# Optimization experiments

Measured on AMD Instinct MI355X. Metric: run time of the kernel, lower is better.

## Reference

```python
import jax, jax.numpy as jnp
import numpy as np

NUM_EXPERTS = 8
PHM_DIM = 4


def setup_inputs() -> dict:
    key = jax.random.key(0)
    k1, k2, k3, k4 = jax.random.split(key, 4)
    bsz, seq, D, O, E, p = 4, 2048, 2048, 2048, NUM_EXPERTS, PHM_DIM
    hidden_states = jax.random.normal(k1, (bsz, seq, D), dtype=jnp.float32)
    gate_w = jax.random.normal(k2, (D, E), dtype=jnp.float32) * 0.02
    phm_rule = jax.random.normal(k3, (E, p, p, p), dtype=jnp.float32) * 0.1
    W = jax.random.normal(k4, (E, p, D // p, O // p), dtype=jnp.float32) * 0.02
    b = jnp.zeros((E, O), dtype=jnp.float32)
    return {"hidden_states": hidden_states, "gate_w": gate_w,
            "phm_rule": phm_rule, "W": W, "b": b}


def reference(hidden_states, gate_w, phm_rule, W, b):
    bsz, seq, dim = hidden_states.shape
    E = gate_w.shape[1]
    x = hidden_states.reshape(-1, dim)                      # [T, D]
    logits = x @ gate_w                                     # [T, E]
    prob = jax.nn.softmax(logits, axis=-1)                  # [T, E]
    gate = jnp.argmax(prob, axis=-1)                        # [T]
    # load-balancing loss
    num_tokens = jnp.sum(jax.nn.one_hot(gate, E, dtype=jnp.int32), axis=0)  # [E]
    f = num_tokens.astype(prob.dtype)
    f = f / jnp.sum(f)
    P = jnp.mean(prob, axis=0)
    balance_loss = E * jnp.sum(P * f)
    # PHM weight per expert: H_e = sum_p kron(phm_rule[e,p], W[e,p]) -> [E, D, O]
    Wfull = jnp.einsum('epab,epij->eaibj', phm_rule, W).reshape(E, dim, -1)
    # dense evaluation of every expert on every token, then top-1 select
    all_out = jnp.einsum('td,edo->teo', x, Wfull) + b[None, :, :]  # [T, E, O]
    tok_prob = jnp.take_along_axis(prob, gate[:, None], axis=1)    # [T, 1]
    out = jnp.take_along_axis(all_out, gate[:, None, None], axis=1)[:, 0, :] * tok_prob
    out = out.reshape(bsz, seq, -1)
    return out, balance_loss, num_tokens
```

## Files before the change

### kernel.cpp

```cpp
#include <hip/hip_runtime.h>
#include <cstdint>
#include <cstddef>

typedef _Float16 f16;
typedef f16 f16x2 __attribute__((ext_vector_type(2)));
typedef f16 f16x4 __attribute__((ext_vector_type(4)));
typedef f16 f16x8 __attribute__((ext_vector_type(8)));
typedef float f32x4 __attribute__((ext_vector_type(4)));

#define NEXP 8
#define BM 128
#define BN 128
#define BK 32

__device__ __forceinline__ void async_cp16(void* lds, const void* gsrc) {
  __builtin_amdgcn_global_load_lds(
      (const __attribute__((address_space(1))) void*)gsrc,
      (__attribute__((address_space(3))) void*)lds, 16, 0, 0);
}

__global__ __launch_bounds__(256) void k_gate(
    const float* __restrict__ x, const float* __restrict__ gw,
    f16* __restrict__ xb, int* __restrict__ gate, float* __restrict__ scale,
    int* __restrict__ cnt, float* __restrict__ probsum, int D)
{
  __shared__ float ps[NEXP];
  __shared__ int pc[NEXP];
  int tid = threadIdx.x, lane = tid & 63, w = tid >> 6;
  if (tid < NEXP) { ps[tid] = 0.f; pc[tid] = 0; }
  __syncthreads();

  int t = blockIdx.x * 4 + w;
  const float* xr = x + (size_t)t * D;
  f16* xbr = xb + (size_t)t * D;

  float acc[NEXP] = {};
  for (int d0 = lane * 4; d0 < D; d0 += 256) {
    float4 v = *(const float4*)(xr + d0);
    f16x4 h; h[0] = (f16)v.x; h[1] = (f16)v.y; h[2] = (f16)v.z; h[3] = (f16)v.w;
    *(f16x4*)(xbr + d0) = h;
    const float* g0 = gw + (size_t)d0 * NEXP;
    float xv[4] = {v.x, v.y, v.z, v.w};
#pragma unroll
    for (int j = 0; j < 4; j++) {
      float4 ga = *(const float4*)(g0 + j * NEXP);
      float4 gb = *(const float4*)(g0 + j * NEXP + 4);
      acc[0] += xv[j] * ga.x; acc[1] += xv[j] * ga.y;
      acc[2] += xv[j] * ga.z; acc[3] += xv[j] * ga.w;
      acc[4] += xv[j] * gb.x; acc[5] += xv[j] * gb.y;
      acc[6] += xv[j] * gb.z; acc[7] += xv[j] * gb.w;
    }
  }
#pragma unroll
  for (int e = 0; e < NEXP; e++) {
    float v = acc[e];
    for (int o = 32; o > 0; o >>= 1) v += __shfl_xor(v, o);
    acc[e] = v;
  }
  if (lane == 0) {
    float m = acc[0]; int g = 0;
#pragma unroll
    for (int e = 1; e < NEXP; e++) if (acc[e] > m) { m = acc[e]; g = e; }
    float pr[NEXP]; float ssum = 0.f;
#pragma unroll
    for (int e = 0; e < NEXP; e++) { pr[e] = expf(acc[e] - m); ssum += pr[e]; }
    float inv = 1.0f / ssum;
#pragma unroll
    for (int e = 0; e < NEXP; e++) atomicAdd(&ps[e], pr[e] * inv);
    atomicAdd(&pc[g], 1);
    gate[t] = g;
    scale[t] = pr[g] * inv;
  }
  __syncthreads();
  if (tid < NEXP) {
    atomicAdd(&probsum[tid], ps[tid]);
    atomicAdd(&cnt[tid], pc[tid]);
  }
}

__global__ __launch_bounds__(256) void k_wfull(
    const float* __restrict__ Wp, const float* __restrict__ rule,
    f16* __restrict__ wt, int Dp, int Op, int D, int O)
{
  int bid = blockIdx.x;
  int it = Dp >> 5, jt = Op >> 5;
  int itile = bid % it; bid /= it;
  int jtile = bid % jt; bid /= jt;
  int b = bid & 3; bid >>= 2;
  int e = bid;
  int i0 = itile * 32, j0 = jtile * 32;

  __shared__ float Wt[4][32][33];
  int tid = threadIdx.x;
  for (int idx = tid; idx < 4096; idx += 256) {
    int p = idx >> 10, rem = idx & 1023, ii = rem >> 5, jj = rem & 31;
    Wt[p][ii][jj] = Wp[(size_t)((e * 4 + p) * Dp + i0 + ii) * Op + j0 + jj];
  }
  float s[4][4];
#pragma unroll
  for (int p = 0; p < 4; p++)
#pragma unroll
    for (int a = 0; a < 4; a++)
      s[p][a] = rule[((e * 4 + p) * 4 + a) * 4 + b];
  __syncthreads();

  int ii = (tid & 15) * 2, jjb = tid >> 4;
#pragma unroll
  for (int a = 0; a < 4; a++) {
#pragma unroll
    for (int jp = 0; jp < 2; jp++) {
      int jj = jjb + jp * 16;
      float v0 = 0.f, v1 = 0.f;
#pragma unroll
      for (int p = 0; p < 4; p++) {
        v0 += s[p][a] * Wt[p][ii][jj];
        v1 += s[p][a] * Wt[p][ii + 1][jj];
      }
      size_t n = (size_t)b * Op + j0 + jj;
      size_t dd = (size_t)a * Dp + i0 + ii;
      f16x2 hv; hv[0] = (f16)v0; hv[1] = (f16)v1;
      *(f16x2*)(wt + ((size_t)e * O + n) * D + dd) = hv;
    }
  }
}

__global__ void k_plan(const int* __restrict__ cnt, const float* __restrict__ probsum,
                       int* __restrict__ offs, int* __restrict__ ndesc,
                       int2* __restrict__ desc, float* __restrict__ otail, int T)
{
  if (threadIdx.x != 0 || blockIdx.x != 0) return;
  int off = 0, nd = 0; float loss = 0.f;
  for (int e = 0; e < NEXP; e++) {
    offs[e] = off;
    int c = cnt[e];
    loss += probsum[e] * (float)c;
    for (int m0 = 0; m0 < c; m0 += BM) { desc[nd] = make_int2(e, m0); nd++; }
    off += c;
  }
  offs[NEXP] = off;
  *ndesc = nd;
  float invT = 1.0f / (float)T;
  otail[0] = (float)NEXP * loss * invT * invT;
  for (int e = 0; e < NEXP; e++) otail[1 + e] = (float)cnt[e];
}

__global__ __launch_bounds__(256) void k_scatter(
    const int* __restrict__ gate, const int* __restrict__ offs,
    int* __restrict__ cursor, int* __restrict__ perm)
{
  int t = blockIdx.x * 256 + threadIdx.x;
  int g = gate[t];
  int lane = threadIdx.x & 63;
  int pos = 0;
#pragma unroll
  for (int e = 0; e < NEXP; e++) {
    unsigned long long mask = __ballot(g == e);
    if (mask == 0ull) continue;
    int leader = __ffsll((unsigned long long)mask) - 1;
    int base = 0;
    if (lane == leader) base = atomicAdd(&cursor[e], (int)__popcll(mask));
    base = __shfl(base, leader);
    if (g == e) {
      int below = (int)__popcll(mask & ((1ull << lane) - 1ull));
      pos = offs[e] + base + below;
    }
  }
  perm[pos] = t;
}

__global__ __launch_bounds__(256) void k_gemm(
    const f16* __restrict__ xb, const f16* __restrict__ wt,
    const float* __restrict__ bias, const int* __restrict__ perm,
    const int* __restrict__ cnt, const int* __restrict__ offs,
    const int* __restrict__ ndesc, const int2* __restrict__ desc,
    const float* __restrict__ scale, float* __restrict__ out, int D, int O)
{
  if ((int)blockIdx.x >= *ndesc) return;
  int2 dsc = desc[blockIdx.x];
  int e = dsc.x, m0 = dsc.y;
  int ce = cnt[e];
  int seg = offs[e];
  int n0 = blockIdx.y * BN;

  __shared__ f16 Al[BM * BK];
  __shared__ f16 Bl[BN * BK];
  __shared__ int tokS[BM];
  __shared__ float scS[BM];

  int tid = threadIdx.x;
  if (tid < BM) {
    int idx = m0 + tid; if (idx > ce - 1) idx = ce - 1;
    int tok = perm[seg + idx];
    tokS[tid] = tok;
    scS[tid] = scale[tok];
  }
  __syncthreads();

  int r = tid >> 2;
  int c = tid & 3;
  const f16* a1 = xb + (size_t)tokS[r] * D + c * 8;
  const f16* a2 = xb + (size_t)tokS[r + 64] * D + c * 8;
  const f16* b1 = wt + ((size_t)e * O + n0 + r) * D + c * 8;
  const f16* b2 = wt + ((size_t)e * O + n0 + r + 64) * D + c * 8;
  f16* la1 = &Al[tid * 8];
  f16* la2 = &Al[2048 + tid * 8];
  f16* lb1 = &Bl[tid * 8];
  f16* lb2 = &Bl[2048 + tid * 8];

  int lane = tid & 63;
  int w = tid >> 6;
  int wm = (w & 1) * 64, wn = (w >> 1) * 64;
  int lr = lane & 15, q = lane >> 4;

  f32x4 acc[4][4] = {};

  int nk = D / BK;
  for (int kk = 0; kk < nk; ++kk) {
    async_cp16(la1, a1 + kk * BK);
    async_cp16(la2, a2 + kk * BK);
    async_cp16(lb1, b1 + kk * BK);
    async_cp16(lb2, b2 + kk * BK);
    __syncthreads();
    f16x8 af[4], bf[4];
#pragma unroll
    for (int mi = 0; mi < 4; mi++)
      af[mi] = *(const f16x8*)&Al[(wm + mi * 16 + lr) * BK + q * 8];
#pragma unroll
    for (int ni = 0; ni < 4; ni++)
      bf[ni] = *(const f16x8*)&Bl[(wn + ni * 16 + lr) * BK + q * 8];
#pragma unroll
    for (int mi = 0; mi < 4; mi++)
#pragma unroll
      for (int ni = 0; ni < 4; ni++)
        acc[mi][ni] = __builtin_amdgcn_mfma_f32_16x16x32_f16(
            af[mi], bf[ni], acc[mi][ni], 0, 0, 0);
    __syncthreads();
  }

  float bv[4];
#pragma unroll
  for (int ni = 0; ni < 4; ni++)
    bv[ni] = bias[(size_t)e * O + n0 + wn + ni * 16 + lr];
#pragma unroll
  for (int mi = 0; mi < 4; mi++) {
#pragma unroll
    for (int rg = 0; rg < 4; rg++) {
      int rl = wm + mi * 16 + q * 4 + rg;
      if (m0 + rl < ce) {
        float s = scS[rl];
        float* orow = out + (size_t)tokS[rl] * O + n0 + wn;
#pragma unroll
        for (int ni = 0; ni < 4; ni++)
          orow[ni * 16 + lr] = (acc[mi][ni][rg] + bv[ni]) * s;
      }
    }
  }
}

extern "C" void kernel_launch(void* const* d_in, const int* in_sizes, int n_in,
                              void* d_out, int out_size, void* d_ws, size_t ws_size,
                              hipStream_t stream)
{
  const float* x    = (const float*)d_in[0];
  const float* gw   = (const float*)d_in[1];
  const float* rule = (const float*)d_in[2];
  const float* W    = (const float*)d_in[3];
  const float* bias = (const float*)d_in[4];
  float* out = (float*)d_out;

  int D = in_sizes[1] / NEXP;
  int O = in_sizes[4] / NEXP;
  int T = in_sizes[0] / D;
  int Dp = D / 4, Op = O / 4;

  uint8_t* ws = (uint8_t*)d_ws;
  size_t off = 0;
  f16* xb = (f16*)(ws + off);  off += (size_t)T * D * 2;
  f16* wt = (f16*)(ws + off);  off += (size_t)NEXP * O * D * 2;
  int*   gate  = (int*)(ws + off);   off += (size_t)T * 4;
  float* scale = (float*)(ws + off); off += (size_t)T * 4;
  int*   perm  = (int*)(ws + off);   off += (size_t)T * 4;
  off = (off + 255) & ~(size_t)255;
  uint8_t* C = ws + off;
  int*   cnt     = (int*)(C + 0);
  float* probsum = (float*)(C + 32);
  int*   cursor  = (int*)(C + 64);
  int*   ndesc   = (int*)(C + 96);
  int*   offs    = (int*)(C + 128);
  int2*  desc    = (int2*)(C + 192);

  hipMemsetAsync(C, 0, 128, stream);

  k_gate<<<T / 4, 256, 0, stream>>>(x, gw, xb, gate, scale, cnt, probsum, D);
  k_wfull<<<NEXP * 4 * (Op / 32) * (Dp / 32), 256, 0, stream>>>(W, rule, wt, Dp, Op, D, O);
  k_plan<<<1, 1, 0, stream>>>(cnt, probsum, offs, ndesc, desc, out + (size_t)T * O, T);
  k_scatter<<<T / 256, 256, 0, stream>>>(gate, offs, cursor, perm);

  int maxdesc = T / BM + NEXP;
  k_gemm<<<dim3(maxdesc, O / BN), 256, 0, stream>>>(
      xb, wt, bias, perm, cnt, offs, ndesc, desc, scale, out, D, O);
}
```

Before: 382.8 us.

## Double-buffer GEMM with swizzled LDS, wider N tile, and fused Kronecker build

```diff
diff --git a/kernel.cpp b/kernel.cpp
--- a/kernel.cpp
+++ b/kernel.cpp
@@ -10,7 +10,7 @@
 
 #define NEXP 8
 #define BM 128
-#define BN 128
+#define BN 256
 #define BK 32
 
 __device__ __forceinline__ void async_cp16(void* lds, const void* gsrc) {
@@ -63,7 +63,7 @@
     for (int e = 1; e < NEXP; e++) if (acc[e] > m) { m = acc[e]; g = e; }
     float pr[NEXP]; float ssum = 0.f;
 #pragma unroll
-    for (int e = 0; e < NEXP; e++) { pr[e] = expf(acc[e] - m); ssum += pr[e]; }
+    for (int e = 0; e < NEXP; e++) { pr[e] = __expf(acc[e] - m); ssum += pr[e]; }
     float inv = 1.0f / ssum;
 #pragma unroll
     for (int e = 0; e < NEXP; e++) atomicAdd(&ps[e], pr[e] * inv);
@@ -86,7 +86,6 @@
   int it = Dp >> 5, jt = Op >> 5;
   int itile = bid % it; bid /= it;
   int jtile = bid % jt; bid /= jt;
-  int b = bid & 3; bid >>= 2;
   int e = bid;
   int i0 = itile * 32, j0 = jtile * 32;
 
@@ -96,30 +95,33 @@
     int p = idx >> 10, rem = idx & 1023, ii = rem >> 5, jj = rem & 31;
     Wt[p][ii][jj] = Wp[(size_t)((e * 4 + p) * Dp + i0 + ii) * Op + j0 + jj];
   }
-  float s[4][4];
-#pragma unroll
-  for (int p = 0; p < 4; p++)
-#pragma unroll
-    for (int a = 0; a < 4; a++)
-      s[p][a] = rule[((e * 4 + p) * 4 + a) * 4 + b];
   __syncthreads();
 
   int ii = (tid & 15) * 2, jjb = tid >> 4;
 #pragma unroll
-  for (int a = 0; a < 4; a++) {
-#pragma unroll
-    for (int jp = 0; jp < 2; jp++) {
-      int jj = jjb + jp * 16;
-      float v0 = 0.f, v1 = 0.f;
-#pragma unroll
-      for (int p = 0; p < 4; p++) {
-        v0 += s[p][a] * Wt[p][ii][jj];
-        v1 += s[p][a] * Wt[p][ii + 1][jj];
+  for (int b = 0; b < 4; b++) {
+    float s[4][4];
+#pragma unroll
+    for (int p = 0; p < 4; p++)
+#pragma unroll
+      for (int a = 0; a < 4; a++)
+        s[p][a] = rule[((e * 4 + p) * 4 + a) * 4 + b];
+#pragma unroll
+    for (int a = 0; a < 4; a++) {
+#pragma unroll
+      for (int jp = 0; jp < 2; jp++) {
+        int jj = jjb + jp * 16;
+        float v0 = 0.f, v1 = 0.f;
+#pragma unroll
+        for (int p = 0; p < 4; p++) {
+          v0 += s[p][a] * Wt[p][ii][jj];
+          v1 += s[p][a] * Wt[p][ii + 1][jj];
+        }
+        size_t n = (size_t)b * Op + j0 + jj;
+        size_t dd = (size_t)a * Dp + i0 + ii;
+        f16x2 hv; hv[0] = (f16)v0; hv[1] = (f16)v1;
+        *(f16x2*)(wt + ((size_t)e * O + n) * D + dd) = hv;
       }
-      size_t n = (size_t)b * Op + j0 + jj;
-      size_t dd = (size_t)a * Dp + i0 + ii;
-      f16x2 hv; hv[0] = (f16)v0; hv[1] = (f16)v1;
-      *(f16x2*)(wt + ((size_t)e * O + n) * D + dd) = hv;
     }
   }
 }
@@ -175,15 +177,15 @@
     const int* __restrict__ ndesc, const int2* __restrict__ desc,
     const float* __restrict__ scale, float* __restrict__ out, int D, int O)
 {
-  if ((int)blockIdx.x >= *ndesc) return;
-  int2 dsc = desc[blockIdx.x];
+  if ((int)blockIdx.y >= *ndesc) return;
+  int2 dsc = desc[blockIdx.y];
   int e = dsc.x, m0 = dsc.y;
   int ce = cnt[e];
   int seg = offs[e];
-  int n0 = blockIdx.y * BN;
-
-  __shared__ f16 Al[BM * BK];
-  __shared__ f16 Bl[BN * BK];
+  int n0 = blockIdx.x * BN;
+
+  __shared__ f16 Al[2][BM * BK];
+  __shared__ f16 Bl[2][BN * BK];
   __shared__ int tokS[BM];
   __shared__ float scS[BM];
 
@@ -198,48 +200,66 @@
 
   int r = tid >> 2;
   int c = tid & 3;
-  const f16* a1 = xb + (size_t)tokS[r] * D + c * 8;
-  const f16* a2 = xb + (size_t)tokS[r + 64] * D + c * 8;
-  const f16* b1 = wt + ((size_t)e * O + n0 + r) * D + c * 8;
-  const f16* b2 = wt + ((size_t)e * O + n0 + r + 64) * D + c * 8;
-  f16* la1 = &Al[tid * 8];
-  f16* la2 = &Al[2048 + tid * 8];
-  f16* lb1 = &Bl[tid * 8];
-  f16* lb2 = &Bl[2048 + tid * 8];
+  int gc = c ^ ((r >> 1) & 3);
+  const f16* a1 = xb + (size_t)tokS[r] * D + gc * 8;
+  const f16* a2 = xb + (size_t)tokS[r + 64] * D + gc * 8;
+  const f16* bp0 = wt + ((size_t)e * O + n0 + r) * D + gc * 8;
+  const f16* bp1 = wt + ((size_t)e * O + n0 + r + 64) * D + gc * 8;
+  const f16* bp2 = wt + ((size_t)e * O + n0 + r + 128) * D + gc * 8;
+  const f16* bp3 = wt + ((size_t)e * O + n0 + r + 192) * D + gc * 8;
 
   int lane = tid & 63;
   int w = tid >> 6;
-  int wm = (w & 1) * 64, wn = (w >> 1) * 64;
+  int wm = (w & 1) * 64, wn = (w >> 1) * 128;
   int lr = lane & 15, q = lane >> 4;
-
-  f32x4 acc[4][4] = {};
-
+  int qs = q ^ ((lr >> 1) & 3);
+
+  f32x4 acc[4][8] = {};
   int nk = D / BK;
+
+#define STAGE(kk, p)                                              \
+  do {                                                            \
+    async_cp16(&Al[(p)][tid * 8], a1 + (kk) * BK);                \
+    async_cp16(&Al[(p)][2048 + tid * 8], a2 + (kk) * BK);         \
+    async_cp16(&Bl[(p)][tid * 8], bp0 + (kk) * BK);               \
+    async_cp16(&Bl[(p)][2048 + tid * 8], bp1 + (kk) * BK);        \
+    async_cp16(&Bl[(p)][4096 + tid * 8], bp2 + (kk) * BK);        \
+    async_cp16(&Bl[(p)][6144 + tid * 8], bp3 + (kk) * BK);        \
+  } while (0)
+
+  STAGE(0, 0);
+  STAGE(1, 1);
+
   for (int kk = 0; kk < nk; ++kk) {
-    async_cp16(la1, a1 + kk * BK);
-    async_cp16(la2, a2 + kk * BK);
-    async_cp16(lb1, b1 + kk * BK);
-    async_cp16(lb2, b2 + kk * BK);
-    __syncthreads();
-    f16x8 af[4], bf[4];
+    int p = kk & 1;
+    if (kk + 1 < nk)
+      asm volatile("s_waitcnt vmcnt(6)\n\ts_barrier" ::: "memory");
+    else
+      asm volatile("s_waitcnt vmcnt(0)\n\ts_barrier" ::: "memory");
+
+    f16x8 af[4], bf[8];
 #pragma unroll
     for (int mi = 0; mi < 4; mi++)
-      af[mi] = *(const f16x8*)&Al[(wm + mi * 16 + lr) * BK + q * 8];
-#pragma unroll
-    for (int ni = 0; ni < 4; ni++)
-      bf[ni] = *(const f16x8*)&Bl[(wn + ni * 16 + lr) * BK + q * 8];
+      af[mi] = *(const f16x8*)&Al[p][(wm + mi * 16 + lr) * BK + qs * 8];
+#pragma unroll
+    for (int ni = 0; ni < 8; ni++)
+      bf[ni] = *(const f16x8*)&Bl[p][(wn + ni * 16 + lr) * BK + qs * 8];
+
+    asm volatile("s_waitcnt lgkmcnt(0)\n\ts_barrier" ::: "memory");
+    if (kk + 2 < nk) STAGE(kk + 2, p);
+
 #pragma unroll
     for (int mi = 0; mi < 4; mi++)
 #pragma unroll
-      for (int ni = 0; ni < 4; ni++)
+      for (int ni = 0; ni < 8; ni++)
         acc[mi][ni] = __builtin_amdgcn_mfma_f32_16x16x32_f16(
             af[mi], bf[ni], acc[mi][ni], 0, 0, 0);
-    __syncthreads();
-  }
-
-  float bv[4];
-#pragma unroll
-  for (int ni = 0; ni < 4; ni++)
+  }
+#undef STAGE
+
+  float bv[8];
+#pragma unroll
+  for (int ni = 0; ni < 8; ni++)
     bv[ni] = bias[(size_t)e * O + n0 + wn + ni * 16 + lr];
 #pragma unroll
   for (int mi = 0; mi < 4; mi++) {
@@ -250,7 +270,7 @@
         float s = scS[rl];
         float* orow = out + (size_t)tokS[rl] * O + n0 + wn;
 #pragma unroll
-        for (int ni = 0; ni < 4; ni++)
+        for (int ni = 0; ni < 8; ni++)
           orow[ni * 16 + lr] = (acc[mi][ni][rg] + bv[ni]) * s;
       }
     }
@@ -292,11 +312,11 @@
   hipMemsetAsync(C, 0, 128, stream);
 
   k_gate<<<T / 4, 256, 0, stream>>>(x, gw, xb, gate, scale, cnt, probsum, D);
-  k_wfull<<<NEXP * 4 * (Op / 32) * (Dp / 32), 256, 0, stream>>>(W, rule, wt, Dp, Op, D, O);
+  k_wfull<<<NEXP * (Op / 32) * (Dp / 32), 256, 0, stream>>>(W, rule, wt, Dp, Op, D, O);
   k_plan<<<1, 1, 0, stream>>>(cnt, probsum, offs, ndesc, desc, out + (size_t)T * O, T);
   k_scatter<<<T / 256, 256, 0, stream>>>(gate, offs, cursor, perm);
 
   int maxdesc = T / BM + NEXP;
-  k_gemm<<<dim3(maxdesc, O / BN), 256, 0, stream>>>(
+  k_gemm<<<dim3(O / BN, maxdesc), 256, 0, stream>>>(
       xb, wt, bias, perm, cnt, offs, ndesc, desc, scale, out, D, O);
 }
```

New measurement: 389.1 us. Within noise of the previous version (+1.6%).
